# Kernel optimization log

Measured on AMD Instinct MI355X. Metric: run time of the kernel, lower is better.

## Reference

```python
import jax, jax.numpy as jnp
import numpy as np


def _bilinear_grid_sample(fea, grid):
    """torch.nn.functional.grid_sample, mode=bilinear, padding_mode=zeros, align_corners=False.
    fea: (B,C,H,W); grid: (B,Hg,Wg,2) with xy in [-1,1]. Returns (B,C,Hg,Wg)."""
    B, C, H, W = fea.shape
    Hg, Wg = grid.shape[1], grid.shape[2]
    gx, gy = grid[..., 0], grid[..., 1]
    # unnormalize (align_corners=False)
    x = ((gx + 1.0) * W - 1.0) * 0.5
    y = ((gy + 1.0) * H - 1.0) * 0.5
    x0 = jnp.floor(x); y0 = jnp.floor(y)
    x1 = x0 + 1.0;     y1 = y0 + 1.0
    wx1 = x - x0; wx0 = 1.0 - wx1
    wy1 = y - y0; wy0 = 1.0 - wy1
    flat = fea.reshape(B, C, H * W)

    def corner(xi, yi, w):
        valid = (xi >= 0) & (xi <= W - 1) & (yi >= 0) & (yi <= H - 1)
        xi_c = jnp.clip(xi, 0, W - 1).astype(jnp.int32)
        yi_c = jnp.clip(yi, 0, H - 1).astype(jnp.int32)
        idx = (yi_c * W + xi_c).reshape(B, 1, Hg * Wg)
        v = jnp.take_along_axis(flat, jnp.broadcast_to(idx, (B, C, Hg * Wg)), axis=2)
        return v * (w * valid.astype(fea.dtype)).reshape(B, 1, Hg * Wg)

    out = (corner(x0, y0, wx0 * wy0) + corner(x1, y0, wx1 * wy0)
           + corner(x0, y1, wx0 * wy1) + corner(x1, y1, wx1 * wy1))
    return out.reshape(B, C, Hg, Wg)


def _conv1d_k1(x, W, b):
    # x: (B,Cin,N), W: (Cout,Cin), b: (Cout,) -> (B,Cout,N)
    return jnp.einsum('oc,bcn->bon', W, x) + b[None, :, None]


def setup_inputs() -> dict:
    key = jax.random.key(0)
    ks = jax.random.split(key, 8)
    B, C, H, W = 4, 16, 90, 160
    N_s, N_anchor, N_y = 8, 200, 20
    scale = 8
    fea = jax.random.normal(ks[0], (B, C, H, W), dtype=jnp.float32)
    sampled_3d_points = jax.random.normal(ks[1], (N_s, B, N_anchor, N_y, 4), dtype=jnp.float32)
    # 2D pixel coords at full resolution: x in [0, W*scale), y in [0, H*scale)
    u = jax.random.uniform(ks[2], (N_s, B, N_anchor, N_y, 2), dtype=jnp.float32)
    points_2d_coord = u * jnp.array([W * scale, H * scale], dtype=jnp.float32)
    W_local = jax.random.normal(ks[3], (16, 16), dtype=jnp.float32) * 0.25
    b_local = jax.random.normal(ks[4], (16,), dtype=jnp.float32) * 0.01
    W_emb = jax.random.normal(ks[5], (256, 4), dtype=jnp.float32) * 0.5
    b_emb = jax.random.normal(ks[6], (256,), dtype=jnp.float32) * 0.01
    return {"fea": fea, "sampled_3d_points": sampled_3d_points,
            "points_2d_coord": points_2d_coord,
            "W_local": W_local, "b_local": b_local,
            "W_emb": W_emb, "b_emb": b_emb, "scale": scale}


def reference(fea, sampled_3d_points, points_2d_coord, W_local, b_local, W_emb, b_emb, scale):
    B, C, H, W = fea.shape
    N_s, _, N_anchor, N_y, _ = points_2d_coord.shape
    # normalize 2D coords to [-1,1] grid
    norm_weight = jnp.array([1.0 / W, 1.0 / H], dtype=fea.dtype)
    ner = (points_2d_coord / scale) * norm_weight * 2.0 - 1.0
    ner = jnp.transpose(ner, (1, 0, 2, 3, 4)).reshape(B, N_s * N_anchor, N_y, 2)
    local_fea = _bilinear_grid_sample(fea, ner)            # (B,C,N_s*N_anchor,N_y)
    local_fea = local_fea.reshape(B, C, -1)                # (B,C,N)
    local_fea = _conv1d_k1(local_fea, W_local, b_local)    # (B,16,N)
    # point embedding: permute(1,4,0,2,3) -> (B,4,N_s,N_anchor,N_y)
    sp = jnp.transpose(sampled_3d_points, (1, 4, 0, 2, 3)).reshape(B, 4, -1)
    embedded_points = _conv1d_k1(sp, W_emb, b_emb)         # (B,256,N)
    return (embedded_points, local_fea)
```

## Files before the change

### kernel.cpp

```cpp
#include <hip/hip_runtime.h>

#define B_    4
#define C_    16
#define H_    90
#define W_    160
#define NS_   8
#define NA_   200
#define NY_   20
#define NPB_  (NS_*NA_*NY_)
#define NPB4_ (NPB_/4)
#define CO_   256
#define EMB_ELEMS ((size_t)B_*CO_*NPB_)
#define SCALE_F 8.0f
#define HW_   (H_*W_)

typedef float f32x4 __attribute__((ext_vector_type(4)));

__device__ __forceinline__ void nt_store4(const float4& v, float4* dst) {
    f32x4 r = { v.x, v.y, v.z, v.w };
    __builtin_nontemporal_store(r, (f32x4*)dst);
}

__global__ __launch_bounds__(256) void fused_local_emb_kernel(
    const float*  __restrict__ fea,
    const float4* __restrict__ sp3d,
    const float2* __restrict__ pc2d,
    const float*  __restrict__ W_local,
    const float*  __restrict__ b_local,
    const float4* __restrict__ W_emb,
    const float*  __restrict__ b_emb,
    float* __restrict__ out)
{
    __shared__ float4 sWe[CO_];
    __shared__ float  sbe[CO_];
    __shared__ float  sWl[256];
    __shared__ float  sbl[16];
    __shared__ float  sPx[256], sPy[256], sPz[256], sPw[256];
    __shared__ float  sV[16*256];

    const int tid = threadIdx.x;
    sWe[tid] = W_emb[tid];
    sbe[tid] = b_emb[tid];
    sWl[tid] = W_local[tid];
    if (tid < 16) sbl[tid] = b_local[tid];

    const int blk  = blockIdx.x;
    const int b    = blk / (NPB_/256);
    const int tile = blk % (NPB_/256);
    const int n    = tile*256 + tid;

    const int s   = n / (NA_*NY_);
    const int rem = n - s*(NA_*NY_);
    const int a   = rem / NY_;
    const int yy  = rem - a*NY_;

    const int pidx = ((s*B_ + b)*NA_ + a)*NY_ + yy;
    const float4 p  = sp3d[pidx];
    const float2 pc = pc2d[pidx];

    sPx[tid] = p.x; sPy[tid] = p.y; sPz[tid] = p.z; sPw[tid] = p.w;

    const float gx = (pc.x / SCALE_F) * (1.0f/(float)W_) * 2.0f - 1.0f;
    const float gy = (pc.y / SCALE_F) * (1.0f/(float)H_) * 2.0f - 1.0f;
    const float xf = ((gx + 1.0f) * (float)W_ - 1.0f) * 0.5f;
    const float yf = ((gy + 1.0f) * (float)H_ - 1.0f) * 0.5f;

    const float x0f = floorf(xf), y0f = floorf(yf);
    const float x1f = x0f + 1.0f, y1f = y0f + 1.0f;
    const float wx1 = xf - x0f, wx0 = 1.0f - wx1;
    const float wy1 = yf - y0f, wy0 = 1.0f - wy1;

    const float vx0 = (x0f >= 0.0f && x0f <= (float)(W_-1)) ? 1.0f : 0.0f;
    const float vx1 = (x1f >= 0.0f && x1f <= (float)(W_-1)) ? 1.0f : 0.0f;
    const float vy0 = (y0f >= 0.0f && y0f <= (float)(H_-1)) ? 1.0f : 0.0f;
    const float vy1 = (y1f >= 0.0f && y1f <= (float)(H_-1)) ? 1.0f : 0.0f;

    const int xi0 = (int)fminf(fmaxf(x0f, 0.0f), (float)(W_-1));
    const int xi1 = (int)fminf(fmaxf(x1f, 0.0f), (float)(W_-1));
    const int yi0 = (int)fminf(fmaxf(y0f, 0.0f), (float)(H_-1));
    const int yi1 = (int)fminf(fmaxf(y1f, 0.0f), (float)(H_-1));

    const float w00 = wx0*wy0*vx0*vy0;
    const float w01 = wx1*wy0*vx1*vy0;
    const float w10 = wx0*wy1*vx0*vy1;
    const float w11 = wx1*wy1*vx1*vy1;

    const int i00 = yi0*W_ + xi0;
    const int i01 = yi0*W_ + xi1;
    const int i10 = yi1*W_ + xi0;
    const int i11 = yi1*W_ + xi1;

    __syncthreads();

    const float* fb = fea + b*(C_*HW_);
    float f00[16], f01[16], f10[16], f11[16];
#pragma unroll
    for (int c = 0; c < 16; ++c) {
        const float* fc = fb + c*HW_;
        f00[c] = fc[i00];
        f01[c] = fc[i01];
        f10[c] = fc[i10];
        f11[c] = fc[i11];
    }

    const int l  = tid & 63;
    const int wv = tid >> 6;

    const float4 PX = ((const float4*)sPx)[l];
    const float4 PY = ((const float4*)sPy)[l];
    const float4 PZ = ((const float4*)sPz)[l];
    const float4 PW = ((const float4*)sPw)[l];

    float4* eo4 = (float4*)(out + (size_t)b*CO_*NPB_ + tile*256);
#pragma unroll
    for (int oi = 0; oi < 64; ++oi) {
        const int o = wv*64 + oi;
        const float4 w = sWe[o];
        const float bb = sbe[o];
        float4 r;
        r.x = fmaf(w.w, PW.x, fmaf(w.z, PZ.x, fmaf(w.y, PY.x, fmaf(w.x, PX.x, bb))));
        r.y = fmaf(w.w, PW.y, fmaf(w.z, PZ.y, fmaf(w.y, PY.y, fmaf(w.x, PX.y, bb))));
        r.z = fmaf(w.w, PW.z, fmaf(w.z, PZ.z, fmaf(w.y, PY.z, fmaf(w.x, PX.z, bb))));
        r.w = fmaf(w.w, PW.w, fmaf(w.z, PZ.w, fmaf(w.y, PY.w, fmaf(w.x, PX.w, bb))));
        nt_store4(r, &eo4[o*NPB4_ + l]);
    }

    float v[16];
#pragma unroll
    for (int c = 0; c < 16; ++c)
        v[c] = w00*f00[c] + w01*f01[c] + w10*f10[c] + w11*f11[c];
#pragma unroll
    for (int c = 0; c < 16; ++c)
        sV[c*256 + tid] = v[c];

    __syncthreads();

    float4 acc[4];
#pragma unroll
    for (int k = 0; k < 4; ++k) {
        const float bk = sbl[4*wv + k];
        acc[k].x = bk; acc[k].y = bk; acc[k].z = bk; acc[k].w = bk;
    }
#pragma unroll
    for (int c = 0; c < 16; ++c) {
        const float4 sv = ((const float4*)(sV + c*256))[l];
#pragma unroll
        for (int k = 0; k < 4; ++k) {
            const float wl = sWl[(4*wv + k)*16 + c];
            acc[k].x = fmaf(wl, sv.x, acc[k].x);
            acc[k].y = fmaf(wl, sv.y, acc[k].y);
            acc[k].z = fmaf(wl, sv.z, acc[k].z);
            acc[k].w = fmaf(wl, sv.w, acc[k].w);
        }
    }
    float4* lo4 = (float4*)(out + EMB_ELEMS + (size_t)b*16*NPB_ + tile*256);
#pragma unroll
    for (int k = 0; k < 4; ++k)
        nt_store4(acc[k], &lo4[(4*wv + k)*NPB4_ + l]);
}

extern "C" void kernel_launch(void* const* d_in, const int* in_sizes, int n_in,
                              void* d_out, int out_size, void* d_ws, size_t ws_size,
                              hipStream_t stream) {
    const float* fea     = (const float*)d_in[0];
    const float4* sp3d   = (const float4*)d_in[1];
    const float2* pc2d   = (const float2*)d_in[2];
    const float* W_local = (const float*)d_in[3];
    const float* b_local = (const float*)d_in[4];
    const float4* W_emb  = (const float4*)d_in[5];
    const float* b_emb   = (const float*)d_in[6];

    dim3 grid(B_ * (NPB_/256));
    dim3 block(256);
    fused_local_emb_kernel<<<grid, block, 0, stream>>>(
        fea, sp3d, pc2d, W_local, b_local, W_emb, b_emb, (float*)d_out);
}
```

Measured before the change: 37.99 us.

## Pre-transpose feature map to channels-last for vectorized bilinear gathers

```diff
diff --git a/kernel.cpp b/kernel.cpp
--- a/kernel.cpp
+++ b/kernel.cpp
@@ -13,6 +13,7 @@
 #define EMB_ELEMS ((size_t)B_*CO_*NPB_)
 #define SCALE_F 8.0f
 #define HW_   (H_*W_)
+#define WS_NEEDED ((size_t)B_*HW_*C_*4)
 
 typedef float f32x4 __attribute__((ext_vector_type(4)));
 
@@ -21,8 +22,30 @@
     __builtin_nontemporal_store(r, (f32x4*)dst);
 }
 
+__global__ __launch_bounds__(256) void transpose_fea_kernel(
+    const float* __restrict__ fea, float* __restrict__ ws)
+{
+    const int t = blockIdx.x*256 + threadIdx.x;
+    const int b = t / HW_;
+    const int p = t - b*HW_;
+    float4 o[4];
+#pragma unroll
+    for (int j = 0; j < 4; ++j) {
+#pragma unroll
+        for (int k = 0; k < 4; ++k) {
+            const int c = j*4 + k;
+            ((float*)&o[j])[k] = fea[(size_t)b*C_*HW_ + c*HW_ + p];
+        }
+    }
+    float4* dst = (float4*)ws + (size_t)t*4;
+#pragma unroll
+    for (int j = 0; j < 4; ++j) dst[j] = o[j];
+}
+
+template <bool TRANSPOSED>
 __global__ __launch_bounds__(256) void fused_local_emb_kernel(
     const float*  __restrict__ fea,
+    const float*  __restrict__ feat,
     const float4* __restrict__ sp3d,
     const float2* __restrict__ pc2d,
     const float*  __restrict__ W_local,
@@ -92,15 +115,26 @@
 
     __syncthreads();
 
-    const float* fb = fea + b*(C_*HW_);
     float f00[16], f01[16], f10[16], f11[16];
-#pragma unroll
-    for (int c = 0; c < 16; ++c) {
-        const float* fc = fb + c*HW_;
-        f00[c] = fc[i00];
-        f01[c] = fc[i01];
-        f10[c] = fc[i10];
-        f11[c] = fc[i11];
+    if (TRANSPOSED) {
+        const float4* wb = (const float4*)feat + (size_t)b*HW_*4;
+#pragma unroll
+        for (int j = 0; j < 4; ++j) {
+            *(float4*)&f00[4*j] = wb[(size_t)i00*4 + j];
+            *(float4*)&f01[4*j] = wb[(size_t)i01*4 + j];
+            *(float4*)&f10[4*j] = wb[(size_t)i10*4 + j];
+            *(float4*)&f11[4*j] = wb[(size_t)i11*4 + j];
+        }
+    } else {
+        const float* fb = fea + b*(C_*HW_);
+#pragma unroll
+        for (int c = 0; c < 16; ++c) {
+            const float* fc = fb + c*HW_;
+            f00[c] = fc[i00];
+            f01[c] = fc[i01];
+            f10[c] = fc[i10];
+            f11[c] = fc[i11];
+        }
     }
 
     const int l  = tid & 63;
@@ -170,8 +204,15 @@
     const float4* W_emb  = (const float4*)d_in[5];
     const float* b_emb   = (const float*)d_in[6];
 
+    dim3 block(256);
     dim3 grid(B_ * (NPB_/256));
-    dim3 block(256);
-    fused_local_emb_kernel<<<grid, block, 0, stream>>>(
-        fea, sp3d, pc2d, W_local, b_local, W_emb, b_emb, (float*)d_out);
-}
+
+    if (ws_size >= WS_NEEDED) {
+        transpose_fea_kernel<<<dim3(B_*HW_/256), block, 0, stream>>>(fea, (float*)d_ws);
+        fused_local_emb_kernel<true><<<grid, block, 0, stream>>>(
+            fea, (const float*)d_ws, sp3d, pc2d, W_local, b_local, W_emb, b_emb, (float*)d_out);
+    } else {
+        fused_local_emb_kernel<false><<<grid, block, 0, stream>>>(
+            fea, nullptr, sp3d, pc2d, W_local, b_local, W_emb, b_emb, (float*)d_out);
+    }
+}
```

Result: slower. 40.50 us (+6.6%).

## Split embedding and local sampling into separate block roles in one launch

Applied to the files above, without the earlier changes.

```diff
diff --git a/kernel.cpp b/kernel.cpp
--- a/kernel.cpp
+++ b/kernel.cpp
@@ -14,6 +14,10 @@
 #define SCALE_F 8.0f
 #define HW_   (H_*W_)
 
+#define EMB_BLOCKS 256
+#define LOC_BLOCKS 500
+#define TOTAL_BLOCKS (EMB_BLOCKS + LOC_BLOCKS)
+
 typedef float f32x4 __attribute__((ext_vector_type(4)));
 
 __device__ __forceinline__ void nt_store4(const float4& v, float4* dst) {
@@ -21,7 +25,7 @@
     __builtin_nontemporal_store(r, (f32x4*)dst);
 }
 
-__global__ __launch_bounds__(256) void fused_local_emb_kernel(
+__global__ __launch_bounds__(320) void fused_local_emb_kernel(
     const float*  __restrict__ fea,
     const float4* __restrict__ sp3d,
     const float2* __restrict__ pc2d,
@@ -31,132 +35,141 @@
     const float*  __restrict__ b_emb,
     float* __restrict__ out)
 {
-    __shared__ float4 sWe[CO_];
-    __shared__ float  sbe[CO_];
-    __shared__ float  sWl[256];
-    __shared__ float  sbl[16];
-    __shared__ float  sPx[256], sPy[256], sPz[256], sPw[256];
-    __shared__ float  sV[16*256];
+    __shared__ float sWl[256];
+    __shared__ float sbl[16];
+    __shared__ float sV[16*256];
 
     const int tid = threadIdx.x;
-    sWe[tid] = W_emb[tid];
-    sbe[tid] = b_emb[tid];
-    sWl[tid] = W_local[tid];
-    if (tid < 16) sbl[tid] = b_local[tid];
+    const int idx = blockIdx.x;
 
-    const int blk  = blockIdx.x;
-    const int b    = blk / (NPB_/256);
-    const int tile = blk % (NPB_/256);
-    const int n    = tile*256 + tid;
+    if (idx < EMB_BLOCKS) {
+        const int b  = idx >> 6;
+        const int oc = idx & 63;
+        const int o0 = oc*4;
 
-    const int s   = n / (NA_*NY_);
-    const int rem = n - s*(NA_*NY_);
-    const int a   = rem / NY_;
-    const int yy  = rem - a*NY_;
+        float4 w[4]; float bb[4];
+#pragma unroll
+        for (int k = 0; k < 4; ++k) { w[k] = W_emb[o0+k]; bb[k] = b_emb[o0+k]; }
 
-    const int pidx = ((s*B_ + b)*NA_ + a)*NY_ + yy;
-    const float4 p  = sp3d[pidx];
-    const float2 pc = pc2d[pidx];
+        const float4* pb = sp3d + b*(NA_*NY_);
+        float4* e4 = (float4*)(out + (size_t)b*CO_*NPB_ + (size_t)o0*NPB_);
 
-    sPx[tid] = p.x; sPy[tid] = p.y; sPz[tid] = p.z; sPw[tid] = p.w;
+#pragma unroll 5
+        for (int i = 0; i < 25; ++i) {
+            const int g  = i*320 + tid;
+            const int s  = g / 1000;
+            const int gi = g - s*1000;
+            const float4* pp = pb + s*(B_*NA_*NY_) + gi*4;
+            const float4 p0 = pp[0], p1 = pp[1], p2 = pp[2], p3 = pp[3];
+#pragma unroll
+            for (int k = 0; k < 4; ++k) {
+                float4 r;
+                r.x = fmaf(w[k].w,p0.w, fmaf(w[k].z,p0.z, fmaf(w[k].y,p0.y, fmaf(w[k].x,p0.x, bb[k]))));
+                r.y = fmaf(w[k].w,p1.w, fmaf(w[k].z,p1.z, fmaf(w[k].y,p1.y, fmaf(w[k].x,p1.x, bb[k]))));
+                r.z = fmaf(w[k].w,p2.w, fmaf(w[k].z,p2.z, fmaf(w[k].y,p2.y, fmaf(w[k].x,p2.x, bb[k]))));
+                r.w = fmaf(w[k].w,p3.w, fmaf(w[k].z,p3.z, fmaf(w[k].y,p3.y, fmaf(w[k].x,p3.x, bb[k]))));
+                nt_store4(r, &e4[(size_t)k*NPB4_ + g]);
+            }
+        }
+        return;
+    }
 
-    const float gx = (pc.x / SCALE_F) * (1.0f/(float)W_) * 2.0f - 1.0f;
-    const float gy = (pc.y / SCALE_F) * (1.0f/(float)H_) * 2.0f - 1.0f;
-    const float xf = ((gx + 1.0f) * (float)W_ - 1.0f) * 0.5f;
-    const float yf = ((gy + 1.0f) * (float)H_ - 1.0f) * 0.5f;
+    const int lid  = idx - EMB_BLOCKS;
+    const bool act = (tid < 256);
+    const int l  = tid & 63;
+    const int wv = tid >> 6;
 
-    const float x0f = floorf(xf), y0f = floorf(yf);
-    const float x1f = x0f + 1.0f, y1f = y0f + 1.0f;
-    const float wx1 = xf - x0f, wx0 = 1.0f - wx1;
-    const float wy1 = yf - y0f, wy0 = 1.0f - wy1;
+    const int b    = lid / 125;
+    const int tile = lid - b*125;
 
-    const float vx0 = (x0f >= 0.0f && x0f <= (float)(W_-1)) ? 1.0f : 0.0f;
-    const float vx1 = (x1f >= 0.0f && x1f <= (float)(W_-1)) ? 1.0f : 0.0f;
-    const float vy0 = (y0f >= 0.0f && y0f <= (float)(H_-1)) ? 1.0f : 0.0f;
-    const float vy1 = (y1f >= 0.0f && y1f <= (float)(H_-1)) ? 1.0f : 0.0f;
+    if (act) {
+        sWl[tid] = W_local[tid];
+        if (tid < 16) sbl[tid] = b_local[tid];
 
-    const int xi0 = (int)fminf(fmaxf(x0f, 0.0f), (float)(W_-1));
-    const int xi1 = (int)fminf(fmaxf(x1f, 0.0f), (float)(W_-1));
-    const int yi0 = (int)fminf(fmaxf(y0f, 0.0f), (float)(H_-1));
-    const int yi1 = (int)fminf(fmaxf(y1f, 0.0f), (float)(H_-1));
+        const int n   = tile*256 + tid;
+        const int s   = n / (NA_*NY_);
+        const int rem = n - s*(NA_*NY_);
+        const int a   = rem / NY_;
+        const int yy  = rem - a*NY_;
 
-    const float w00 = wx0*wy0*vx0*vy0;
-    const float w01 = wx1*wy0*vx1*vy0;
-    const float w10 = wx0*wy1*vx0*vy1;
-    const float w11 = wx1*wy1*vx1*vy1;
+        const float2 pc = pc2d[((s*B_ + b)*NA_ + a)*NY_ + yy];
 
-    const int i00 = yi0*W_ + xi0;
-    const int i01 = yi0*W_ + xi1;
-    const int i10 = yi1*W_ + xi0;
-    const int i11 = yi1*W_ + xi1;
+        const float gx = (pc.x / SCALE_F) * (1.0f/(float)W_) * 2.0f - 1.0f;
+        const float gy = (pc.y / SCALE_F) * (1.0f/(float)H_) * 2.0f - 1.0f;
+        const float xf = ((gx + 1.0f) * (float)W_ - 1.0f) * 0.5f;
+        const float yf = ((gy + 1.0f) * (float)H_ - 1.0f) * 0.5f;
+
+        const float x0f = floorf(xf), y0f = floorf(yf);
+        const float x1f = x0f + 1.0f, y1f = y0f + 1.0f;
+        const float wx1 = xf - x0f, wx0 = 1.0f - wx1;
+        const float wy1 = yf - y0f, wy0 = 1.0f - wy1;
+
+        const float vx0 = (x0f >= 0.0f && x0f <= (float)(W_-1)) ? 1.0f : 0.0f;
+        const float vx1 = (x1f >= 0.0f && x1f <= (float)(W_-1)) ? 1.0f : 0.0f;
+        const float vy0 = (y0f >= 0.0f && y0f <= (float)(H_-1)) ? 1.0f : 0.0f;
+        const float vy1 = (y1f >= 0.0f && y1f <= (float)(H_-1)) ? 1.0f : 0.0f;
+
+        const int xi0 = (int)fminf(fmaxf(x0f, 0.0f), (float)(W_-1));
+        const int xi1 = (int)fminf(fmaxf(x1f, 0.0f), (float)(W_-1));
+        const int yi0 = (int)fminf(fmaxf(y0f, 0.0f), (float)(H_-1));
+        const int yi1 = (int)fminf(fmaxf(y1f, 0.0f), (float)(H_-1));
+
+        const float w00 = wx0*wy0*vx0*vy0;
+        const float w01 = wx1*wy0*vx1*vy0;
+        const float w10 = wx0*wy1*vx0*vy1;
+        const float w11 = wx1*wy1*vx1*vy1;
+
+        const int i00 = yi0*W_ + xi0;
+        const int i01 = yi0*W_ + xi1;
+        const int i10 = yi1*W_ + xi0;
+        const int i11 = yi1*W_ + xi1;
+
+        const float* fb = fea + b*(C_*HW_);
+        float f00[16], f01[16], f10[16], f11[16];
+#pragma unroll
+        for (int c = 0; c < 16; ++c) {
+            const float* fc = fb + c*HW_;
+            f00[c] = fc[i00];
+            f01[c] = fc[i01];
+            f10[c] = fc[i10];
+            f11[c] = fc[i11];
+        }
+
+        float v[16];
+#pragma unroll
+        for (int c = 0; c < 16; ++c)
+            v[c] = w00*f00[c] + w01*f01[c] + w10*f10[c] + w11*f11[c];
+#pragma unroll
+        for (int c = 0; c < 16; ++c)
+            sV[c*256 + tid] = v[c];
+    }
 
     __syncthreads();
 
-    const float* fb = fea + b*(C_*HW_);
-    float f00[16], f01[16], f10[16], f11[16];
-#pragma unroll
-    for (int c = 0; c < 16; ++c) {
-        const float* fc = fb + c*HW_;
-        f00[c] = fc[i00];
-        f01[c] = fc[i01];
-        f10[c] = fc[i10];
-        f11[c] = fc[i11];
-    }
-
-    const int l  = tid & 63;
-    const int wv = tid >> 6;
-
-    const float4 PX = ((const float4*)sPx)[l];
-    const float4 PY = ((const float4*)sPy)[l];
-    const float4 PZ = ((const float4*)sPz)[l];
-    const float4 PW = ((const float4*)sPw)[l];
-
-    float4* eo4 = (float4*)(out + (size_t)b*CO_*NPB_ + tile*256);
-#pragma unroll
-    for (int oi = 0; oi < 64; ++oi) {
-        const int o = wv*64 + oi;
-        const float4 w = sWe[o];
-        const float bb = sbe[o];
-        float4 r;
-        r.x = fmaf(w.w, PW.x, fmaf(w.z, PZ.x, fmaf(w.y, PY.x, fmaf(w.x, PX.x, bb))));
-        r.y = fmaf(w.w, PW.y, fmaf(w.z, PZ.y, fmaf(w.y, PY.y, fmaf(w.x, PX.y, bb))));
-        r.z = fmaf(w.w, PW.z, fmaf(w.z, PZ.z, fmaf(w.y, PY.z, fmaf(w.x, PX.z, bb))));
-        r.w = fmaf(w.w, PW.w, fmaf(w.z, PZ.w, fmaf(w.y, PY.w, fmaf(w.x, PX.w, bb))));
-        nt_store4(r, &eo4[o*NPB4_ + l]);
-    }
-
-    float v[16];
-#pragma unroll
-    for (int c = 0; c < 16; ++c)
-        v[c] = w00*f00[c] + w01*f01[c] + w10*f10[c] + w11*f11[c];
-#pragma unroll
-    for (int c = 0; c < 16; ++c)
-        sV[c*256 + tid] = v[c];
-
-    __syncthreads();
-
-    float4 acc[4];
-#pragma unroll
-    for (int k = 0; k < 4; ++k) {
-        const float bk = sbl[4*wv + k];
-        acc[k].x = bk; acc[k].y = bk; acc[k].z = bk; acc[k].w = bk;
-    }
-#pragma unroll
-    for (int c = 0; c < 16; ++c) {
-        const float4 sv = ((const float4*)(sV + c*256))[l];
+    if (act) {
+        float4 acc[4];
 #pragma unroll
         for (int k = 0; k < 4; ++k) {
-            const float wl = sWl[(4*wv + k)*16 + c];
-            acc[k].x = fmaf(wl, sv.x, acc[k].x);
-            acc[k].y = fmaf(wl, sv.y, acc[k].y);
-            acc[k].z = fmaf(wl, sv.z, acc[k].z);
-            acc[k].w = fmaf(wl, sv.w, acc[k].w);
+            const float bk = sbl[4*wv + k];
+            acc[k].x = bk; acc[k].y = bk; acc[k].z = bk; acc[k].w = bk;
         }
+#pragma unroll
+        for (int c = 0; c < 16; ++c) {
+            const float4 sv = ((const float4*)(sV + c*256))[l];
+#pragma unroll
+            for (int k = 0; k < 4; ++k) {
+                const float wl = sWl[(4*wv + k)*16 + c];
+                acc[k].x = fmaf(wl, sv.x, acc[k].x);
+                acc[k].y = fmaf(wl, sv.y, acc[k].y);
+                acc[k].z = fmaf(wl, sv.z, acc[k].z);
+                acc[k].w = fmaf(wl, sv.w, acc[k].w);
+            }
+        }
+        float4* lo4 = (float4*)(out + EMB_ELEMS + (size_t)b*16*NPB_ + tile*256);
+#pragma unroll
+        for (int k = 0; k < 4; ++k)
+            nt_store4(acc[k], &lo4[(4*wv + k)*NPB4_ + l]);
     }
-    float4* lo4 = (float4*)(out + EMB_ELEMS + (size_t)b*16*NPB_ + tile*256);
-#pragma unroll
-    for (int k = 0; k < 4; ++k)
-        nt_store4(acc[k], &lo4[(4*wv + k)*NPB4_ + l]);
 }
 
 extern "C" void kernel_launch(void* const* d_in, const int* in_sizes, int n_in,
@@ -170,8 +183,8 @@
     const float4* W_emb  = (const float4*)d_in[5];
     const float* b_emb   = (const float*)d_in[6];
 
-    dim3 grid(B_ * (NPB_/256));
-    dim3 block(256);
+    dim3 grid(TOTAL_BLOCKS);
+    dim3 block(320);
     fused_local_emb_kernel<<<grid, block, 0, stream>>>(
         fea, sp3d, pc2d, W_local, b_local, W_emb, b_emb, (float*)d_out);
 }
```

Result: slower. 46.37 us (+22.0%).
